# Kernel optimization log

Measured on AMD Instinct MI355X. Metric: run time of the kernel, lower is better.

The kernel has to match this reference:

```python
import jax, jax.numpy as jnp
import numpy as np

H = 128          # num_hidden
NIN = 256        # num_in (2*H: edge feat + gathered node feat)
B, L, K = 2, 2048, 48
SCALE = 30.0
LN_EPS = 1e-5


def _layer_norm(x, g, b):
    mu = jnp.mean(x, axis=-1, keepdims=True)
    var = jnp.var(x, axis=-1, keepdims=True)
    return g * (x - mu) * jax.lax.rsqrt(var + LN_EPS) + b


def _gather_nodes(nodes, idx):
    # nodes: [B,L,C], idx: [B,L,K] -> [B,L,K,C]
    return jax.vmap(lambda n, i: n[i])(nodes, idx)


def _gelu(x):
    return jax.nn.gelu(x, approximate=False)  # torch GELU default (erf)


def setup_inputs() -> dict:
    key = jax.random.key(0)
    ks = jax.random.split(key, 24)
    p = lambda k, shp: (jax.random.normal(k, shp, jnp.float32) * 0.05)
    inp = {
        "h_V": jax.random.normal(ks[0], (B, L, H), jnp.float32),
        "h_E": jax.random.normal(ks[1], (B, L, K, H), jnp.float32),
        "E_idx": jax.random.randint(ks[2], (B, L, K), 0, L),
        "mask_V": jnp.ones((B, L), jnp.float32),
        "mask_attend": jnp.ones((B, L, K), jnp.float32),
        # node-message MLP W1-W2-W3
        "W1": p(ks[3], (H + NIN, H)), "b1": jnp.zeros((H,), jnp.float32),
        "W2": p(ks[4], (H, H)), "b2": jnp.zeros((H,), jnp.float32),
        "W3": p(ks[5], (H, H)), "b3": jnp.zeros((H,), jnp.float32),
        # edge-update MLP W11-W12-W13
        "W11": p(ks[6], (H + NIN, H)), "b11": jnp.zeros((H,), jnp.float32),
        "W12": p(ks[7], (H, H)), "b12": jnp.zeros((H,), jnp.float32),
        "W13": p(ks[8], (H, H)), "b13": jnp.zeros((H,), jnp.float32),
        # layer norms
        "g1": jnp.ones((H,), jnp.float32), "be1": jnp.zeros((H,), jnp.float32),
        "g2": jnp.ones((H,), jnp.float32), "be2": jnp.zeros((H,), jnp.float32),
        "g3": jnp.ones((H,), jnp.float32), "be3": jnp.zeros((H,), jnp.float32),
        # position-wise FFN (H -> 4H -> H)
        "W_in": p(ks[9], (H, 4 * H)), "b_in": jnp.zeros((4 * H,), jnp.float32),
        "W_out": p(ks[10], (4 * H, H)), "b_out": jnp.zeros((H,), jnp.float32),
    }
    return inp


def reference(h_V, h_E, E_idx, mask_V, mask_attend,
              W1, b1, W2, b2, W3, b3,
              W11, b11, W12, b12, W13, b13,
              g1, be1, g2, be2, g3, be3,
              W_in, b_in, W_out, b_out):
    # ---- node update: gather neighbors, concat, 3-layer MLP, masked sum ----
    h_nb = _gather_nodes(h_V, E_idx)                       # [B,L,K,H]
    h_EV = jnp.concatenate(
        [jnp.broadcast_to(h_V[:, :, None, :], h_nb.shape), h_E, h_nb], axis=-1)
    h_msg = _gelu(h_EV @ W1 + b1)
    h_msg = _gelu(h_msg @ W2 + b2)
    h_msg = h_msg @ W3 + b3                                # [B,L,K,H]
    h_msg = mask_attend[..., None] * h_msg
    dh = jnp.sum(h_msg, axis=-2) / SCALE                   # [B,L,H]
    h_V = _layer_norm(h_V + dh, g1, be1)
    # ---- position-wise FFN + residual ----
    dh = _gelu(h_V @ W_in + b_in) @ W_out + b_out
    h_V = _layer_norm(h_V + dh, g2, be2)
    h_V = mask_V[..., None] * h_V
    # ---- edge update ----
    h_nb = _gather_nodes(h_V, E_idx)
    h_EV = jnp.concatenate(
        [jnp.broadcast_to(h_V[:, :, None, :], h_nb.shape), h_E, h_nb], axis=-1)
    h_msg = _gelu(h_EV @ W11 + b11)
    h_msg = _gelu(h_msg @ W12 + b12)
    h_msg = h_msg @ W13 + b13
    h_E = _layer_norm(h_E + h_msg, g3, be3)
    return h_V, h_E
```

## Files before the change

kernel.cpp:

```cpp
#include <hip/hip_runtime.h>
#include <hip/hip_bf16.h>
#include <math.h>

#define Hdim 128
#define Kn 48
#define NN 4096
#define FFH 512
#define LN_EPS 1e-5f

typedef __attribute__((ext_vector_type(8))) short bf16x8;
typedef __attribute__((ext_vector_type(4))) float floatx4;
typedef unsigned short ushort_t;

#define CMA(row, col) ((((col) >> 3) * 784) + ((row) << 4) + (((col)&7) << 1))

__device__ __forceinline__ float gelu_f(float x) {
    float x2 = x * x;
    float u = x * fmaf(x2, -0.1029454f, -2.3022081f);
    return x * __builtin_amdgcn_rcpf(1.0f + exp2f(u));
}

__device__ __forceinline__ ushort_t f2bf(float f) {
    __hip_bfloat16 h = __float2bfloat16(f);
    return *reinterpret_cast<ushort_t*>(&h);
}
__device__ __forceinline__ float bf2f(ushort_t h) {
    union { unsigned u; float f; } v;
    v.u = ((unsigned)h) << 16;
    return v.f;
}

__global__ __launch_bounds__(256) void convert_all(
    const float* __restrict__ W1, const float* __restrict__ W11,
    const float* __restrict__ W2, const float* __restrict__ W3,
    const float* __restrict__ W12, const float* __restrict__ W13,
    const float* __restrict__ W_in, const float* __restrict__ W_out,
    const float* __restrict__ hV, const float* __restrict__ b1,
    ushort_t* __restrict__ Wt1m, ushort_t* __restrict__ Wt11m,
    ushort_t* __restrict__ Wt11a, ushort_t* __restrict__ Wt2,
    ushort_t* __restrict__ Wt3, ushort_t* __restrict__ Wt12,
    ushort_t* __restrict__ Wt13, ushort_t* __restrict__ WtIn,
    ushort_t* __restrict__ WtOut, ushort_t* __restrict__ hVbf,
    float* __restrict__ selfA) {
    __shared__ __align__(16) char cmem[8448];
    const int b = blockIdx.x, t = threadIdx.x;

    if (b < 272) {
        const float* src;
        ushort_t* dst;
        int K, C, rowOff, tile;
        if (b < 32)       { src = W1;   dst = Wt1m;  K = 256; C = 128; rowOff = 128; tile = b; }
        else if (b < 64)  { src = W11;  dst = Wt11m; K = 256; C = 128; rowOff = 128; tile = b - 32; }
        else if (b < 80)  { src = W11;  dst = Wt11a; K = 128; C = 128; rowOff = 0;   tile = b - 64; }
        else if (b < 96)  { src = W2;   dst = Wt2;   K = 128; C = 128; rowOff = 0;   tile = b - 80; }
        else if (b < 112) { src = W3;   dst = Wt3;   K = 128; C = 128; rowOff = 0;   tile = b - 96; }
        else if (b < 128) { src = W12;  dst = Wt12;  K = 128; C = 128; rowOff = 0;   tile = b - 112; }
        else if (b < 144) { src = W13;  dst = Wt13;  K = 128; C = 128; rowOff = 0;   tile = b - 128; }
        else if (b < 208) { src = W_in; dst = WtIn;  K = 128; C = 512; rowOff = 0;   tile = b - 144; }
        else              { src = W_out;dst = WtOut; K = 512; C = 128; rowOff = 0;   tile = b - 208; }
        const int tpr = C >> 5;
        const int tk = tile / tpr, tn = tile % tpr;
        const int tr0 = tk * 32, tc0 = tn * 32;
        const int KD32 = K >> 5;
        float (*s)[33] = (float(*)[33])cmem;
#pragma unroll
        for (int i = 0; i < 4; ++i) {
            int r = (t >> 5) + i * 8, c = t & 31;
            s[r][c] = src[(size_t)(rowOff + tr0 + r) * C + tc0 + c];
        }
        __syncthreads();
        if (t < 128) {
            int n_loc = t >> 2, kc0 = (t & 3) * 8;
            int n = tc0 + n_loc, k = tr0 + kc0;
            ushort_t o[8];
#pragma unroll
            for (int e = 0; e < 8; ++e) o[e] = f2bf(s[kc0 + e][n_loc]);
            size_t idx = (size_t)((n >> 4) * KD32 + (k >> 5)) * 512 +
                         ((k >> 3) & 3) * 128 + (n & 15) * 8;
            *(uint4*)(dst + idx) = *(const uint4*)o;
        }
    } else if (b < 528) {
        int i = (b - 272) * 2048 + t * 8;
        float4 a = *(const float4*)(hV + (size_t)i);
        float4 c = *(const float4*)(hV + (size_t)i + 4);
        ushort_t o[8] = {f2bf(a.x), f2bf(a.y), f2bf(a.z), f2bf(a.w),
                         f2bf(c.x), f2bf(c.y), f2bf(c.z), f2bf(c.w)};
        *(uint4*)(hVbf + (size_t)i) = *(const uint4*)o;
    } else {
        float (*xs)[Hdim] = (float(*)[Hdim])cmem;
        const int grp = t >> 7, o = t & 127;
        const int nb0 = (b - 528) * 16;
#pragma unroll
        for (int n = 0; n < 8; ++n)
            xs[grp * 8 + n][o] = hV[(size_t)(nb0 + grp * 8 + n) * Hdim + o];
        __syncthreads();
        float acc[8];
        const float bo = b1[o];
#pragma unroll
        for (int n = 0; n < 8; ++n) acc[n] = bo;
        for (int i = 0; i < Hdim; i += 4) {
            const float w0 = W1[(i + 0) * Hdim + o];
            const float w1 = W1[(i + 1) * Hdim + o];
            const float w2 = W1[(i + 2) * Hdim + o];
            const float w3 = W1[(i + 3) * Hdim + o];
#pragma unroll
            for (int n = 0; n < 8; ++n) {
                const float4 v = *(const float4*)&xs[grp * 8 + n][i];
                acc[n] = fmaf(v.x, w0, acc[n]);
                acc[n] = fmaf(v.y, w1, acc[n]);
                acc[n] = fmaf(v.z, w2, acc[n]);
                acc[n] = fmaf(v.w, w3, acc[n]);
            }
        }
#pragma unroll
        for (int n = 0; n < 8; ++n)
            selfA[(size_t)(nb0 + grp * 8 + n) * Hdim + o] = acc[n];
    }
}

template <int MODE>
__global__ __launch_bounds__(256, 4) void edge_mlp(
    const float* __restrict__ hV, const float* __restrict__ hE,
    const int* __restrict__ Eidx, const float* __restrict__ maskAtt,
    const float* __restrict__ selfA, const ushort_t* __restrict__ hVbf,
    const ushort_t* __restrict__ WtA, const ushort_t* __restrict__ WtB,
    const ushort_t* __restrict__ WtC, const float* __restrict__ bias2,
    const float* __restrict__ bias3, const float* __restrict__ gamma,
    const float* __restrict__ beta, float* __restrict__ outp) {
    __shared__ __align__(16) char T0[32 * 784];
    __shared__ __align__(16) char T1[16 * 784];
    __shared__ int idx_s[Kn];
    __shared__ float dh_s[128];
    __shared__ float rsum[Kn][4], rsum2[Kn][4];
    __shared__ float mu_s[Kn], rs_s[Kn];
    __shared__ float rw[8];
    char* T2 = T0 + 16 * 784;

    const int tid = threadIdx.x;
    const int lane = tid & 63;
    const int w = tid >> 6;
    const int l15 = lane & 15, l4 = lane >> 4;
    const int n = blockIdx.x;
    const int n0 = w * 32;
    const int bbase = (n >> 11) << 11;
    const int abase = l4 * 784 + l15 * 16;
    const int fbase = l4 * 128 + l15 * 8;

    if (tid < Kn) idx_s[tid] = Eidx[(size_t)n * Kn + tid];
    {
        const float4* src = (const float4*)(hE + (size_t)n * Kn * Hdim);
#pragma unroll
        for (int it = 0; it < 6; ++it) {
            int i = tid + it * 256;
            float4 v = src[i];
            int row = i >> 5, j = i & 31;
            unsigned lo = f2bf(v.x) | ((unsigned)f2bf(v.y) << 16);
            unsigned hi = f2bf(v.z) | ((unsigned)f2bf(v.w) << 16);
            *(uint2*)(T0 + (j >> 1) * 784 + row * 16 + (j & 1) * 8) =
                make_uint2(lo, hi);
        }
    }
    __syncthreads();
#pragma unroll
    for (int it = 0; it < 3; ++it) {
        int i = tid + it * 256;
        int row = i >> 4, c = i & 15;
        uint4 v =
            *(const uint4*)(hVbf + (size_t)(bbase + idx_s[row]) * Hdim + c * 8);
        *(uint4*)(T0 + (16 + c) * 784 + row * 16) = v;
    }
    __syncthreads();

    floatx4 acc[3][2];
#pragma unroll
    for (int mt = 0; mt < 3; ++mt)
#pragma unroll
        for (int nt = 0; nt < 2; ++nt) acc[mt][nt] = (floatx4)0.0f;

#pragma unroll
    for (int kk = 0; kk < 8; ++kk) {
        bf16x8 a[3], bb[2];
#pragma unroll
        for (int mt = 0; mt < 3; ++mt)
            a[mt] = *(const bf16x8*)(T0 + abase + mt * 256 + kk * 3136);
#pragma unroll
        for (int nt = 0; nt < 2; ++nt)
            bb[nt] = *(const bf16x8*)(WtA + ((w * 2 + nt) * 8 + kk) * 512 +
                                      fbase);
#pragma unroll
        for (int mt = 0; mt < 3; ++mt)
#pragma unroll
            for (int nt = 0; nt < 2; ++nt)
                acc[mt][nt] = __builtin_amdgcn_mfma_f32_16x16x32_bf16(
                    a[mt], bb[nt], acc[mt][nt], 0, 0, 0);
    }
    {
        float sA[2];
#pragma unroll
        for (int nt = 0; nt < 2; ++nt)
            sA[nt] = selfA[(size_t)n * Hdim + n0 + nt * 16 + l15];
#pragma unroll
        for (int mt = 0; mt < 3; ++mt)
#pragma unroll
            for (int nt = 0; nt < 2; ++nt) {
                const int col = n0 + nt * 16 + l15;
#pragma unroll
                for (int r = 0; r < 4; ++r) {
                    float v = gelu_f(acc[mt][nt][r] + sA[nt]);
                    int row = mt * 16 + l4 * 4 + r;
                    *(ushort_t*)(T1 + CMA(row, col)) = f2bf(v);
                }
            }
    }
    __syncthreads();

    {
        float bv[2];
#pragma unroll
        for (int nt = 0; nt < 2; ++nt) bv[nt] = bias2[n0 + nt * 16 + l15];
#pragma unroll
        for (int mt = 0; mt < 3; ++mt)
#pragma unroll
            for (int nt = 0; nt < 2; ++nt)
                acc[mt][nt] = (floatx4){bv[nt], bv[nt], bv[nt], bv[nt]};
    }
#pragma unroll
    for (int kk = 0; kk < 4; ++kk) {
        bf16x8 a[3], bb[2];
#pragma unroll
        for (int mt = 0; mt < 3; ++mt)
            a[mt] = *(const bf16x8*)(T1 + abase + mt * 256 + kk * 3136);
#pragma unroll
        for (int nt = 0; nt < 2; ++nt)
            bb[nt] = *(const bf16x8*)(WtB + ((w * 2 + nt) * 4 + kk) * 512 +
                                      fbase);
#pragma unroll
        for (int mt = 0; mt < 3; ++mt)
#pragma unroll
            for (int nt = 0; nt < 2; ++nt)
                acc[mt][nt] = __builtin_amdgcn_mfma_f32_16x16x32_bf16(
                    a[mt], bb[nt], acc[mt][nt], 0, 0, 0);
    }
    __syncthreads();
#pragma unroll
    for (int mt = 0; mt < 3; ++mt)
#pragma unroll
        for (int nt = 0; nt < 2; ++nt) {
            const int col = n0 + nt * 16 + l15;
#pragma unroll
            for (int r = 0; r < 4; ++r) {
                float v = gelu_f(acc[mt][nt][r]);
                int row = mt * 16 + l4 * 4 + r;
                *(ushort_t*)(T2 + CMA(row, col)) = f2bf(v);
            }
        }
    __syncthreads();

    {
        float bv[2];
#pragma unroll
        for (int nt = 0; nt < 2; ++nt) bv[nt] = bias3[n0 + nt * 16 + l15];
#pragma unroll
        for (int mt = 0; mt < 3; ++mt)
#pragma unroll
            for (int nt = 0; nt < 2; ++nt)
                acc[mt][nt] = (floatx4){bv[nt], bv[nt], bv[nt], bv[nt]};
    }
#pragma unroll
    for (int kk = 0; kk < 4; ++kk) {
        bf16x8 a[3], bb[2];
#pragma unroll
        for (int mt = 0; mt < 3; ++mt)
            a[mt] = *(const bf16x8*)(T2 + abase + mt * 256 + kk * 3136);
#pragma unroll
        for (int nt = 0; nt < 2; ++nt)
            bb[nt] = *(const bf16x8*)(WtC + ((w * 2 + nt) * 4 + kk) * 512 +
                                      fbase);
#pragma unroll
        for (int mt = 0; mt < 3; ++mt)
#pragma unroll
            for (int nt = 0; nt < 2; ++nt)
                acc[mt][nt] = __builtin_amdgcn_mfma_f32_16x16x32_bf16(
                    a[mt], bb[nt], acc[mt][nt], 0, 0, 0);
    }

    if (MODE == 0) {
        float mav[3][4];
#pragma unroll
        for (int mt = 0; mt < 3; ++mt)
#pragma unroll
            for (int r = 0; r < 4; ++r)
                mav[mt][r] = maskAtt[(size_t)n * Kn + mt * 16 + l4 * 4 + r];
#pragma unroll
        for (int nt = 0; nt < 2; ++nt) {
            float c = 0.0f;
#pragma unroll
            for (int mt = 0; mt < 3; ++mt)
#pragma unroll
                for (int r = 0; r < 4; ++r)
                    c = fmaf(mav[mt][r], acc[mt][nt][r], c);
            c += __shfl_xor(c, 16);
            c += __shfl_xor(c, 32);
            if (l4 == 0) dh_s[n0 + nt * 16 + l15] = c;
        }
        __syncthreads();
        float x = 0.0f;
        if (tid < 128) {
            x = hV[(size_t)n * Hdim + tid] + dh_s[tid] * (1.0f / 30.0f);
            float s = x, s2 = x * x;
#pragma unroll
            for (int off = 32; off > 0; off >>= 1) {
                s += __shfl_xor(s, off);
                s2 += __shfl_xor(s2, off);
            }
            if (lane == 0) {
                rw[w * 2] = s;
                rw[w * 2 + 1] = s2;
            }
        }
        __syncthreads();
        if (tid < 128) {
            const float ts = rw[0] + rw[2], ts2 = rw[1] + rw[3];
            const float mu = ts * (1.0f / Hdim);
            const float var = ts2 * (1.0f / Hdim) - mu * mu;
            const float rs = rsqrtf(var + LN_EPS);
            outp[(size_t)n * Hdim + tid] =
                gamma[tid] * (x - mu) * rs + beta[tid];
        }
    } else {
        float xv[3][2][4];
#pragma unroll
        for (int mt = 0; mt < 3; ++mt)
#pragma unroll
            for (int nt = 0; nt < 2; ++nt) {
                const int col = n0 + nt * 16 + l15;
#pragma unroll
                for (int r = 0; r < 4; ++r) {
                    int row = mt * 16 + l4 * 4 + r;
                    ushort_t hv = *(const ushort_t*)(T0 + CMA(row, col));
                    xv[mt][nt][r] = acc[mt][nt][r] + bf2f(hv);
                }
            }
#pragma unroll
        for (int mt = 0; mt < 3; ++mt)
#pragma unroll
            for (int r = 0; r < 4; ++r) {
                float s = xv[mt][0][r] + xv[mt][1][r];
                float s2 = xv[mt][0][r] * xv[mt][0][r] +
                           xv[mt][1][r] * xv[mt][1][r];
#pragma unroll
                for (int off = 1; off < 16; off <<= 1) {
                    s += __shfl_xor(s, off);
                    s2 += __shfl_xor(s2, off);
                }
                if (l15 == 0) {
                    int row = mt * 16 + l4 * 4 + r;
                    rsum[row][w] = s;
                    rsum2[row][w] = s2;
                }
            }
        __syncthreads();
        if (tid < Kn) {
            float s = rsum[tid][0] + rsum[tid][1] + rsum[tid][2] + rsum[tid][3];
            float s2 =
                rsum2[tid][0] + rsum2[tid][1] + rsum2[tid][2] + rsum2[tid][3];
            float mu = s * (1.0f / Hdim);
            float var = s2 * (1.0f / Hdim) - mu * mu;
            mu_s[tid] = mu;
            rs_s[tid] = rsqrtf(var + LN_EPS);
        }
        __syncthreads();
        float gv[2], bv[2];
#pragma unroll
        for (int nt = 0; nt < 2; ++nt) {
            gv[nt] = gamma[n0 + nt * 16 + l15];
            bv[nt] = beta[n0 + nt * 16 + l15];
        }
#pragma unroll
        for (int mt = 0; mt < 3; ++mt)
#pragma unroll
            for (int nt = 0; nt < 2; ++nt) {
                const int col = n0 + nt * 16 + l15;
#pragma unroll
                for (int r = 0; r < 4; ++r) {
                    int row = mt * 16 + l4 * 4 + r;
                    float y = gv[nt] * (xv[mt][nt][r] - mu_s[row]) *
                                  rs_s[row] + bv[nt];
                    outp[((size_t)n * Kn + row) * Hdim + col] = y;
                }
            }
    }
}

__global__ __launch_bounds__(512) void ffn_mfma(
    const float* __restrict__ hV2, const ushort_t* __restrict__ WtIn,
    const float* __restrict__ b_in, const ushort_t* __restrict__ WtOut,
    const float* __restrict__ b_out, const ushort_t* __restrict__ Wt11a,
    const float* __restrict__ b11, const float* __restrict__ g2,
    const float* __restrict__ be2, const float* __restrict__ maskV,
    float* __restrict__ outp, ushort_t* __restrict__ outb,
    float* __restrict__ selfA2) {
    __shared__ __align__(16) char XF[16 * 272];
    __shared__ __align__(16) char HF[64 * 272];
    __shared__ float rsF[16][8], rs2F[16][8], muF[16], rstdF[16];

    const int tid = threadIdx.x;
    const int lane = tid & 63;
    const int w = tid >> 6;
    const int l15 = lane & 15, l4 = lane >> 4;
    const int rg0 = blockIdx.x * 16;
    const int abase = l4 * 272 + l15 * 16;
    const int fbase = l4 * 128 + l15 * 8;

    {
        const float4* src = (const float4*)(hV2 + (size_t)rg0 * Hdim);
        int i = tid;
        float4 v = src[i];
        int row = i >> 5, j = i & 31;
        unsigned lo = f2bf(v.x) | ((unsigned)f2bf(v.y) << 16);
        unsigned hi = f2bf(v.z) | ((unsigned)f2bf(v.w) << 16);
        *(uint2*)(XF + (j >> 1) * 272 + row * 16 + (j & 1) * 8) =
            make_uint2(lo, hi);
    }
    __syncthreads();
    {
        floatx4 a1[4];
#pragma unroll
        for (int j = 0; j < 4; ++j) {
            float bv = b_in[(w * 4 + j) * 16 + l15];
            a1[j] = (floatx4){bv, bv, bv, bv};
        }
#pragma unroll
        for (int kk = 0; kk < 4; ++kk) {
            bf16x8 af = *(const bf16x8*)(XF + abase + kk * 1088);
#pragma unroll
            for (int j = 0; j < 4; ++j) {
                bf16x8 bf = *(const bf16x8*)(WtIn +
                             ((w * 4 + j) * 4 + kk) * 512 + fbase);
                a1[j] = __builtin_amdgcn_mfma_f32_16x16x32_bf16(af, bf, a1[j],
                                                                0, 0, 0);
            }
        }
#pragma unroll
        for (int j = 0; j < 4; ++j) {
            const int col = (w * 4 + j) * 16 + l15;
#pragma unroll
            for (int r = 0; r < 4; ++r) {
                int row = l4 * 4 + r;
                *(ushort_t*)(HF + ((col >> 3) * 272) + row * 16 +
                             ((col & 7) << 1)) = f2bf(gelu_f(a1[j][r]));
            }
        }
    }
    __syncthreads();
    floatx4 o2;
    {
        float bv = b_out[w * 16 + l15];
        o2 = (floatx4){bv, bv, bv, bv};
    }
#pragma unroll
    for (int kk = 0; kk < 16; ++kk) {
        bf16x8 af = *(const bf16x8*)(HF + abase + kk * 1088);
        bf16x8 bf = *(const bf16x8*)(WtOut + (w * 16 + kk) * 512 + fbase);
        o2 = __builtin_amdgcn_mfma_f32_16x16x32_bf16(af, bf, o2, 0, 0, 0);
    }
    const int colw = w * 16 + l15;
    float xv[4];
#pragma unroll
    for (int r = 0; r < 4; ++r)
        xv[r] = hV2[(size_t)(rg0 + l4 * 4 + r) * Hdim + colw] + o2[r];
#pragma unroll
    for (int r = 0; r < 4; ++r) {
        float s = xv[r], s2 = xv[r] * xv[r];
#pragma unroll
        for (int off = 1; off < 16; off <<= 1) {
            s += __shfl_xor(s, off);
            s2 += __shfl_xor(s2, off);
        }
        if (l15 == 0) {
            rsF[l4 * 4 + r][w] = s;
            rs2F[l4 * 4 + r][w] = s2;
        }
    }
    __syncthreads();
    if (tid < 16) {
        float s = 0.0f, s2 = 0.0f;
#pragma unroll
        for (int q = 0; q < 8; ++q) { s += rsF[tid][q]; s2 += rs2F[tid][q]; }
        float mu = s * (1.0f / Hdim);
        float var = s2 * (1.0f / Hdim) - mu * mu;
        muF[tid] = mu;
        rstdF[tid] = rsqrtf(var + LN_EPS);
    }
    __syncthreads();
    {
        float gvv = g2[colw], bvv = be2[colw];
#pragma unroll
        for (int r = 0; r < 4; ++r) {
            int row = l4 * 4 + r;
            float y = (gvv * (xv[r] - muF[row]) * rstdF[row] + bvv) *
                      maskV[rg0 + row];
            ushort_t yb = f2bf(y);
            outp[(size_t)(rg0 + row) * Hdim + colw] = y;
            outb[(size_t)(rg0 + row) * Hdim + colw] = yb;
            *(ushort_t*)(XF + ((colw >> 3) * 272) + row * 16 +
                         ((colw & 7) << 1)) = yb;
        }
    }
    __syncthreads();
    {
        float bv = b11[colw];
        floatx4 sa = (floatx4){bv, bv, bv, bv};
#pragma unroll
        for (int kk = 0; kk < 4; ++kk) {
            bf16x8 af = *(const bf16x8*)(XF + abase + kk * 1088);
            bf16x8 bf = *(const bf16x8*)(Wt11a + (w * 4 + kk) * 512 + fbase);
            sa = __builtin_amdgcn_mfma_f32_16x16x32_bf16(af, bf, sa, 0, 0, 0);
        }
#pragma unroll
        for (int r = 0; r < 4; ++r)
            selfA2[(size_t)(rg0 + l4 * 4 + r) * Hdim + colw] = sa[r];
    }
}

extern "C" void kernel_launch(void* const* d_in, const int* in_sizes, int n_in,
                              void* d_out, int out_size, void* d_ws,
                              size_t ws_size, hipStream_t stream) {
    const float* hV = (const float*)d_in[0];
    const float* hE = (const float*)d_in[1];
    const int* Eidx = (const int*)d_in[2];
    const float* maskV = (const float*)d_in[3];
    const float* maskAtt = (const float*)d_in[4];
    const float* W1 = (const float*)d_in[5];
    const float* b1 = (const float*)d_in[6];
    const float* W2 = (const float*)d_in[7];
    const float* b2 = (const float*)d_in[8];
    const float* W3 = (const float*)d_in[9];
    const float* b3 = (const float*)d_in[10];
    const float* W11 = (const float*)d_in[11];
    const float* b11 = (const float*)d_in[12];
    const float* W12 = (const float*)d_in[13];
    const float* b12 = (const float*)d_in[14];
    const float* W13 = (const float*)d_in[15];
    const float* b13 = (const float*)d_in[16];
    const float* g1 = (const float*)d_in[17];
    const float* be1 = (const float*)d_in[18];
    const float* g2 = (const float*)d_in[19];
    const float* be2 = (const float*)d_in[20];
    const float* g3 = (const float*)d_in[21];
    const float* be3 = (const float*)d_in[22];
    const float* W_in = (const float*)d_in[23];
    const float* b_in = (const float*)d_in[24];
    const float* W_out = (const float*)d_in[25];
    const float* b_out = (const float*)d_in[26];

    float* out_hV = (float*)d_out;
    float* out_hE = out_hV + (size_t)NN * Hdim;
    float* ws = (float*)d_ws;
    float* hV2 = ws;
    float* selfA = ws + 524288;
    ushort_t* u = (ushort_t*)(ws + 1048576);
    ushort_t* hVbf = u;
    ushort_t* outVbf = u + 524288;
    ushort_t* Wt1m = u + 1048576;
    ushort_t* Wt11m = u + 1081344;
    ushort_t* Wt11a = u + 1114112;
    ushort_t* Wt2 = u + 1130496;
    ushort_t* Wt3 = u + 1146880;
    ushort_t* Wt12 = u + 1163264;
    ushort_t* Wt13 = u + 1179648;
    ushort_t* WtIn = u + 1196032;
    ushort_t* WtOut = u + 1261568;

    convert_all<<<784, 256, 0, stream>>>(W1, W11, W2, W3, W12, W13, W_in,
                                         W_out, hV, b1, Wt1m, Wt11m, Wt11a,
                                         Wt2, Wt3, Wt12, Wt13, WtIn, WtOut,
                                         hVbf, selfA);
    edge_mlp<0><<<NN, 256, 0, stream>>>(hV, hE, Eidx, maskAtt, selfA, hVbf,
                                        Wt1m, Wt2, Wt3, b2, b3, g1, be1, hV2);
    ffn_mfma<<<NN / 16, 512, 0, stream>>>(hV2, WtIn, b_in, WtOut, b_out,
                                          Wt11a, b11, g2, be2, maskV, out_hV,
                                          outVbf, selfA);
    edge_mlp<1><<<NN, 256, 0, stream>>>(nullptr, hE, Eidx, nullptr, selfA,
                                        outVbf, Wt11m, Wt12, Wt13, b12, b13,
                                        g3, be3, out_hE);
}
```

Baseline: 330.0 us.

## Shrink edge MLP shared memory for higher occupancy and halve FFN block rows

The edge MLP kernel reuses a single upper half of the T0 tile for both intermediate activation buffers and packs the small reduction arrays into one aliased aux buffer. This cuts shared memory per block so the launch bound can rise from 4 to 6 blocks per CU, at the cost of an extra barrier before the first overwrite. Separately, the FFN kernel now processes 8 rows per 256-thread block instead of 16 rows per 512 threads, padding the MFMA tiles with zeros. This doubles the grid size for better CU coverage but wastes half of each MFMA tile.

```diff
diff --git a/kernel.cpp b/kernel.cpp
--- a/kernel.cpp
+++ b/kernel.cpp
@@ -119,7 +119,7 @@
 }
 
 template <int MODE>
-__global__ __launch_bounds__(256, 4) void edge_mlp(
+__global__ __launch_bounds__(256, 6) void edge_mlp(
     const float* __restrict__ hV, const float* __restrict__ hE,
     const int* __restrict__ Eidx, const float* __restrict__ maskAtt,
     const float* __restrict__ selfA, const ushort_t* __restrict__ hVbf,
@@ -128,13 +128,14 @@
     const float* __restrict__ bias3, const float* __restrict__ gamma,
     const float* __restrict__ beta, float* __restrict__ outp) {
     __shared__ __align__(16) char T0[32 * 784];
-    __shared__ __align__(16) char T1[16 * 784];
-    __shared__ int idx_s[Kn];
-    __shared__ float dh_s[128];
-    __shared__ float rsum[Kn][4], rsum2[Kn][4];
-    __shared__ float mu_s[Kn], rs_s[Kn];
-    __shared__ float rw[8];
-    char* T2 = T0 + 16 * 784;
+    __shared__ __align__(16) char aux[1728];
+    int* idx_s = (int*)aux;
+    float* dh_s = (float*)(aux + 192);
+    float* rw = (float*)(aux + 704);
+    float2* rsums = (float2*)(aux + 192);
+    float* mu_s = (float*)(aux + 192);
+    float* rs_s = (float*)(aux + 384);
+    char* THI = T0 + 16 * 784;
 
     const int tid = threadIdx.x;
     const int lane = tid & 63;
@@ -194,6 +195,7 @@
                 acc[mt][nt] = __builtin_amdgcn_mfma_f32_16x16x32_bf16(
                     a[mt], bb[nt], acc[mt][nt], 0, 0, 0);
     }
+    __syncthreads();
     {
         float sA[2];
 #pragma unroll
@@ -208,7 +210,7 @@
                 for (int r = 0; r < 4; ++r) {
                     float v = gelu_f(acc[mt][nt][r] + sA[nt]);
                     int row = mt * 16 + l4 * 4 + r;
-                    *(ushort_t*)(T1 + CMA(row, col)) = f2bf(v);
+                    *(ushort_t*)(THI + CMA(row, col)) = f2bf(v);
                 }
             }
     }
@@ -229,7 +231,7 @@
         bf16x8 a[3], bb[2];
 #pragma unroll
         for (int mt = 0; mt < 3; ++mt)
-            a[mt] = *(const bf16x8*)(T1 + abase + mt * 256 + kk * 3136);
+            a[mt] = *(const bf16x8*)(THI + abase + mt * 256 + kk * 3136);
 #pragma unroll
         for (int nt = 0; nt < 2; ++nt)
             bb[nt] = *(const bf16x8*)(WtB + ((w * 2 + nt) * 4 + kk) * 512 +
@@ -251,7 +253,7 @@
             for (int r = 0; r < 4; ++r) {
                 float v = gelu_f(acc[mt][nt][r]);
                 int row = mt * 16 + l4 * 4 + r;
-                *(ushort_t*)(T2 + CMA(row, col)) = f2bf(v);
+                *(ushort_t*)(THI + CMA(row, col)) = f2bf(v);
             }
         }
     __syncthreads();
@@ -271,7 +273,7 @@
         bf16x8 a[3], bb[2];
 #pragma unroll
         for (int mt = 0; mt < 3; ++mt)
-            a[mt] = *(const bf16x8*)(T2 + abase + mt * 256 + kk * 3136);
+            a[mt] = *(const bf16x8*)(THI + abase + mt * 256 + kk * 3136);
 #pragma unroll
         for (int nt = 0; nt < 2; ++nt)
             bb[nt] = *(const bf16x8*)(WtC + ((w * 2 + nt) * 4 + kk) * 512 +
@@ -355,15 +357,15 @@
                 }
                 if (l15 == 0) {
                     int row = mt * 16 + l4 * 4 + r;
-                    rsum[row][w] = s;
-                    rsum2[row][w] = s2;
+                    rsums[row * 4 + w] = make_float2(s, s2);
                 }
             }
         __syncthreads();
         if (tid < Kn) {
-            float s = rsum[tid][0] + rsum[tid][1] + rsum[tid][2] + rsum[tid][3];
-            float s2 =
-                rsum2[tid][0] + rsum2[tid][1] + rsum2[tid][2] + rsum2[tid][3];
+            float2 p0 = rsums[tid * 4 + 0], p1 = rsums[tid * 4 + 1];
+            float2 p2 = rsums[tid * 4 + 2], p3 = rsums[tid * 4 + 3];
+            float s = p0.x + p1.x + p2.x + p3.x;
+            float s2 = p0.y + p1.y + p2.y + p3.y;
             float mu = s * (1.0f / Hdim);
             float var = s2 * (1.0f / Hdim) - mu * mu;
             mu_s[tid] = mu;
@@ -392,7 +394,7 @@
     }
 }
 
-__global__ __launch_bounds__(512) void ffn_mfma(
+__global__ __launch_bounds__(256) void ffn_mfma(
     const float* __restrict__ hV2, const ushort_t* __restrict__ WtIn,
     const float* __restrict__ b_in, const ushort_t* __restrict__ WtOut,
     const float* __restrict__ b_out, const ushort_t* __restrict__ Wt11a,
@@ -402,124 +404,158 @@
     float* __restrict__ selfA2) {
     __shared__ __align__(16) char XF[16 * 272];
     __shared__ __align__(16) char HF[64 * 272];
-    __shared__ float rsF[16][8], rs2F[16][8], muF[16], rstdF[16];
+    __shared__ float rsF[8][4], rs2F[8][4], muF[8], rstdF[8];
 
     const int tid = threadIdx.x;
     const int lane = tid & 63;
     const int w = tid >> 6;
     const int l15 = lane & 15, l4 = lane >> 4;
-    const int rg0 = blockIdx.x * 16;
-    const int abase = l4 * 272 + l15 * 16;
+    const int rg0 = blockIdx.x * 8;
     const int fbase = l4 * 128 + l15 * 8;
 
     {
         const float4* src = (const float4*)(hV2 + (size_t)rg0 * Hdim);
-        int i = tid;
-        float4 v = src[i];
-        int row = i >> 5, j = i & 31;
+        float4 v = src[tid];
+        int row = tid >> 5, j = tid & 31;
         unsigned lo = f2bf(v.x) | ((unsigned)f2bf(v.y) << 16);
         unsigned hi = f2bf(v.z) | ((unsigned)f2bf(v.w) << 16);
         *(uint2*)(XF + (j >> 1) * 272 + row * 16 + (j & 1) * 8) =
             make_uint2(lo, hi);
+        if (tid < 128) {
+            int c = tid >> 3, rr = tid & 7;
+            *(uint4*)(XF + c * 272 + (8 + rr) * 16) = make_uint4(0, 0, 0, 0);
+        }
     }
     __syncthreads();
     {
-        floatx4 a1[4];
-#pragma unroll
-        for (int j = 0; j < 4; ++j) {
-            float bv = b_in[(w * 4 + j) * 16 + l15];
+        floatx4 a1[8];
+#pragma unroll
+        for (int j = 0; j < 8; ++j) {
+            float bv = b_in[(w * 8 + j) * 16 + l15];
             a1[j] = (floatx4){bv, bv, bv, bv};
         }
 #pragma unroll
         for (int kk = 0; kk < 4; ++kk) {
-            bf16x8 af = *(const bf16x8*)(XF + abase + kk * 1088);
-#pragma unroll
-            for (int j = 0; j < 4; ++j) {
+            bf16x8 af = *(const bf16x8*)(XF + (kk * 4 + l4) * 272 + l15 * 16);
+#pragma unroll
+            for (int j = 0; j < 8; ++j) {
                 bf16x8 bf = *(const bf16x8*)(WtIn +
-                             ((w * 4 + j) * 4 + kk) * 512 + fbase);
+                             ((w * 8 + j) * 4 + kk) * 512 + fbase);
                 a1[j] = __builtin_amdgcn_mfma_f32_16x16x32_bf16(af, bf, a1[j],
                                                                 0, 0, 0);
             }
         }
 #pragma unroll
-        for (int j = 0; j < 4; ++j) {
-            const int col = (w * 4 + j) * 16 + l15;
+        for (int j = 0; j < 8; ++j) {
+            const int col = (w * 8 + j) * 16 + l15;
 #pragma unroll
             for (int r = 0; r < 4; ++r) {
                 int row = l4 * 4 + r;
-                *(ushort_t*)(HF + ((col >> 3) * 272) + row * 16 +
+                *(ushort_t*)(HF + (col >> 3) * 272 + row * 16 +
                              ((col & 7) << 1)) = f2bf(gelu_f(a1[j][r]));
             }
         }
     }
     __syncthreads();
-    floatx4 o2;
-    {
-        float bv = b_out[w * 16 + l15];
-        o2 = (floatx4){bv, bv, bv, bv};
+    floatx4 o2[2];
+#pragma unroll
+    for (int nt = 0; nt < 2; ++nt) {
+        float bv = b_out[(w * 2 + nt) * 16 + l15];
+        o2[nt] = (floatx4){bv, bv, bv, bv};
     }
 #pragma unroll
     for (int kk = 0; kk < 16; ++kk) {
-        bf16x8 af = *(const bf16x8*)(HF + abase + kk * 1088);
-        bf16x8 bf = *(const bf16x8*)(WtOut + (w * 16 + kk) * 512 + fbase);
-        o2 = __builtin_amdgcn_mfma_f32_16x16x32_bf16(af, bf, o2, 0, 0, 0);
-    }
-    const int colw = w * 16 + l15;
-    float xv[4];
-#pragma unroll
-    for (int r = 0; r < 4; ++r)
-        xv[r] = hV2[(size_t)(rg0 + l4 * 4 + r) * Hdim + colw] + o2[r];
+        bf16x8 af = *(const bf16x8*)(HF + (kk * 4 + l4) * 272 + l15 * 16);
+#pragma unroll
+        for (int nt = 0; nt < 2; ++nt) {
+            bf16x8 bf = *(const bf16x8*)(WtOut +
+                         ((w * 2 + nt) * 16 + kk) * 512 + fbase);
+            o2[nt] = __builtin_amdgcn_mfma_f32_16x16x32_bf16(af, bf, o2[nt],
+                                                             0, 0, 0);
+        }
+    }
+    float xv[2][4];
+#pragma unroll
+    for (int nt = 0; nt < 2; ++nt) {
+        const int col = (w * 2 + nt) * 16 + l15;
+#pragma unroll
+        for (int r = 0; r < 4; ++r) {
+            int row = l4 * 4 + r;
+            xv[nt][r] = (l4 < 2)
+                ? hV2[(size_t)(rg0 + row) * Hdim + col] + o2[nt][r] : 0.0f;
+        }
+    }
 #pragma unroll
     for (int r = 0; r < 4; ++r) {
-        float s = xv[r], s2 = xv[r] * xv[r];
+        float s = xv[0][r] + xv[1][r];
+        float s2 = xv[0][r] * xv[0][r] + xv[1][r] * xv[1][r];
 #pragma unroll
         for (int off = 1; off < 16; off <<= 1) {
             s += __shfl_xor(s, off);
             s2 += __shfl_xor(s2, off);
         }
-        if (l15 == 0) {
+        if (l15 == 0 && l4 < 2) {
             rsF[l4 * 4 + r][w] = s;
             rs2F[l4 * 4 + r][w] = s2;
         }
     }
     __syncthreads();
-    if (tid < 16) {
-        float s = 0.0f, s2 = 0.0f;
-#pragma unroll
-        for (int q = 0; q < 8; ++q) { s += rsF[tid][q]; s2 += rs2F[tid][q]; }
+    if (tid < 8) {
+        float s = rsF[tid][0] + rsF[tid][1] + rsF[tid][2] + rsF[tid][3];
+        float s2 = rs2F[tid][0] + rs2F[tid][1] + rs2F[tid][2] + rs2F[tid][3];
         float mu = s * (1.0f / Hdim);
         float var = s2 * (1.0f / Hdim) - mu * mu;
         muF[tid] = mu;
         rstdF[tid] = rsqrtf(var + LN_EPS);
     }
     __syncthreads();
+    if (l4 < 2) {
+#pragma unroll
+        for (int nt = 0; nt < 2; ++nt) {
+            const int col = (w * 2 + nt) * 16 + l15;
+            float gvv = g2[col], bvv = be2[col];
+#pragma unroll
+            for (int r = 0; r < 4; ++r) {
+                int row = l4 * 4 + r;
+                float y = (gvv * (xv[nt][r] - muF[row]) * rstdF[row] + bvv) *
+                          maskV[rg0 + row];
+                ushort_t yb = f2bf(y);
+                outp[(size_t)(rg0 + row) * Hdim + col] = y;
+                outb[(size_t)(rg0 + row) * Hdim + col] = yb;
+                *(ushort_t*)(XF + (col >> 3) * 272 + row * 16 +
+                             ((col & 7) << 1)) = yb;
+            }
+        }
+    }
+    __syncthreads();
     {
-        float gvv = g2[colw], bvv = be2[colw];
-#pragma unroll
-        for (int r = 0; r < 4; ++r) {
-            int row = l4 * 4 + r;
-            float y = (gvv * (xv[r] - muF[row]) * rstdF[row] + bvv) *
-                      maskV[rg0 + row];
-            ushort_t yb = f2bf(y);
-            outp[(size_t)(rg0 + row) * Hdim + colw] = y;
-            outb[(size_t)(rg0 + row) * Hdim + colw] = yb;
-            *(ushort_t*)(XF + ((colw >> 3) * 272) + row * 16 +
-                         ((colw & 7) << 1)) = yb;
-        }
-    }
-    __syncthreads();
-    {
-        float bv = b11[colw];
-        floatx4 sa = (floatx4){bv, bv, bv, bv};
+        floatx4 sa[2];
+#pragma unroll
+        for (int nt = 0; nt < 2; ++nt) {
+            float bv = b11[(w * 2 + nt) * 16 + l15];
+            sa[nt] = (floatx4){bv, bv, bv, bv};
+        }
 #pragma unroll
         for (int kk = 0; kk < 4; ++kk) {
-            bf16x8 af = *(const bf16x8*)(XF + abase + kk * 1088);
-            bf16x8 bf = *(const bf16x8*)(Wt11a + (w * 4 + kk) * 512 + fbase);
-            sa = __builtin_amdgcn_mfma_f32_16x16x32_bf16(af, bf, sa, 0, 0, 0);
-        }
-#pragma unroll
-        for (int r = 0; r < 4; ++r)
-            selfA2[(size_t)(rg0 + l4 * 4 + r) * Hdim + colw] = sa[r];
+            bf16x8 af = *(const bf16x8*)(XF + (kk * 4 + l4) * 272 + l15 * 16);
+#pragma unroll
+            for (int nt = 0; nt < 2; ++nt) {
+                bf16x8 bf = *(const bf16x8*)(Wt11a +
+                             ((w * 2 + nt) * 4 + kk) * 512 + fbase);
+                sa[nt] = __builtin_amdgcn_mfma_f32_16x16x32_bf16(af, bf,
+                                                                 sa[nt], 0, 0, 0);
+            }
+        }
+        if (l4 < 2) {
+#pragma unroll
+            for (int nt = 0; nt < 2; ++nt) {
+                const int col = (w * 2 + nt) * 16 + l15;
+#pragma unroll
+                for (int r = 0; r < 4; ++r)
+                    selfA2[(size_t)(rg0 + l4 * 4 + r) * Hdim + col] =
+                        sa[nt][r];
+            }
+        }
     }
 }
 
@@ -578,9 +614,9 @@
                                          hVbf, selfA);
     edge_mlp<0><<<NN, 256, 0, stream>>>(hV, hE, Eidx, maskAtt, selfA, hVbf,
                                         Wt1m, Wt2, Wt3, b2, b3, g1, be1, hV2);
-    ffn_mfma<<<NN / 16, 512, 0, stream>>>(hV2, WtIn, b_in, WtOut, b_out,
-                                          Wt11a, b11, g2, be2, maskV, out_hV,
-                                          outVbf, selfA);
+    ffn_mfma<<<NN / 8, 256, 0, stream>>>(hV2, WtIn, b_in, WtOut, b_out,
+                                         Wt11a, b11, g2, be2, maskV, out_hV,
+                                         outVbf, selfA);
     edge_mlp<1><<<NN, 256, 0, stream>>>(nullptr, hE, Eidx, nullptr, selfA,
                                         outVbf, Wt11m, Wt12, Wt13, b12, b13,
                                         g3, be3, out_hE);
```

Measured after the change: 348.1 us. +5.5%, slower.
